# Kernel optimization log

Measured on AMD Instinct MI355X. Metric: run time of the kernel, lower is better.

The kernel has to match this reference:

```python
import math
import jax, jax.numpy as jnp
import numpy as np

NUM_HEADS = 16
HEAD_DIM = 64
MAX_POS = 2048  # max_position_embeddings


def setup_inputs() -> dict:
    key = jax.random.key(0)
    ks = jax.random.split(key, 8)
    B, S, H = 2, 2048, 1024
    return {
        "hidden_states": jax.random.normal(ks[0], (B, S, H), jnp.float32),
        "Wq": jax.random.normal(ks[1], (H, H), jnp.float32) * 0.02,
        "bq": jax.random.normal(ks[2], (H,), jnp.float32) * 0.02,
        "Wk": jax.random.normal(ks[3], (H, H), jnp.float32) * 0.02,
        "bk": jax.random.normal(ks[4], (H,), jnp.float32) * 0.02,
        "Wv": jax.random.normal(ks[5], (H, H), jnp.float32) * 0.02,
        "bv": jax.random.normal(ks[6], (H,), jnp.float32) * 0.02,
        "dist_emb": jax.random.normal(ks[7], (2 * MAX_POS - 1, HEAD_DIM), jnp.float32) * 0.02,
    }


def reference(hidden_states, Wq, bq, Wk, bk, Wv, bv, dist_emb):
    B, S, H = hidden_states.shape
    nh, hd = NUM_HEADS, HEAD_DIM
    # projections (nn.Linear: x @ W.T + b), split into heads
    q = (hidden_states @ Wq.T + bq).reshape(B, S, nh, hd)
    k = (hidden_states @ Wk.T + bk).reshape(B, S, nh, hd)
    v = (hidden_states @ Wv.T + bv).reshape(B, S, nh, hd)
    scale = 1.0 / math.sqrt(hd)
    scores = jnp.einsum('bqhd,bkhd->bhqk', q, k) * scale  # [B,H,S,S]
    # relative position embeddings: distance = q_pos - k_pos
    pos = jnp.arange(S)
    distance = pos[:, None] - pos[None, :]          # [S,S]
    pe = dist_emb[MAX_POS - 1 + distance]           # [S,S,hd]
    rel_q = jnp.einsum('bqhd,qkd->bhqk', q, pe) * scale
    rel_k = jnp.einsum('bkhd,qkd->bhqk', k, pe) * scale
    scores = scores + rel_q + rel_k
    probs = jax.nn.softmax(scores, axis=-1)         # dropout p=0.0
    ctx = jnp.einsum('bhqk,bkhd->bqhd', probs, v)
    return ctx.reshape(B, S, nh * hd)
```

## Files before the change

kernel.cpp:

```cpp
#include <hip/hip_runtime.h>
#include <hip/hip_bf16.h>

#define NH 16
#define HD 64
#define SEQ 2048
#define HID 1024
#define MAXP 2048
#define ST_R 68

typedef float f32x4 __attribute__((ext_vector_type(4)));
typedef short bf16x8 __attribute__((ext_vector_type(8)));
typedef unsigned short u16;
typedef unsigned short u16x8 __attribute__((ext_vector_type(8)));

__device__ __forceinline__ u16 f2bf_hw(float x) {
  union { __hip_bfloat16 h; u16 u; } v;
  v.h = __float2bfloat16(x);
  return v.u;
}
__device__ __forceinline__ unsigned pk2(float a, float b) {
  return (unsigned)f2bf_hw(a) | ((unsigned)f2bf_hw(b) << 16);
}
__device__ __forceinline__ float bf2f(u16 h) {
  union { unsigned u; float f; } v; v.u = ((unsigned)h) << 16;
  return v.f;
}

#define SWZ(r, c) ((r) * 64 + ((((c) >> 3) ^ ((r) & 7)) << 3) + ((c) & 7))

__device__ __forceinline__ void async_copy16(void* lds, const void* g) {
  __builtin_amdgcn_global_load_lds(
      (const __attribute__((address_space(1))) unsigned int*)g,
      (__attribute__((address_space(3))) unsigned int*)lds, 16, 0, 0);
}

__global__ __launch_bounds__(256) void cvt_f32_bf16(
    const float* __restrict__ src, u16* __restrict__ dst, int n4) {
  int i = blockIdx.x * 256 + threadIdx.x;
  const int stride = gridDim.x * 256;
  for (; i < n4; i += stride) {
    const float4 v = reinterpret_cast<const float4*>(src)[i];
    uint2 d;
    d.x = pk2(v.x, v.y);
    d.y = pk2(v.z, v.w);
    reinterpret_cast<uint2*>(dst)[i] = d;
  }
}

__global__ __launch_bounds__(256) void proj_mfma(
    const u16* __restrict__ Xb, const u16* __restrict__ W0,
    const u16* __restrict__ W1, const u16* __restrict__ W2,
    const float* __restrict__ b0, const float* __restrict__ b1,
    const float* __restrict__ b2,
    u16* __restrict__ O0, u16* __restrict__ O1, u16* __restrict__ O2) {
  __shared__ u16 sA[128 * 64];
  __shared__ u16 sB[128 * 64];
  const int t = threadIdx.x, lane = t & 63, w = t >> 6;
  const int g = lane >> 4, li = lane & 15;
  const int wsel = blockIdx.x >> 3;
  const int n0 = (blockIdx.x & 7) * 128, m0 = blockIdx.y * 128;
  const u16* Wb = wsel == 0 ? W0 : (wsel == 1 ? W1 : W2);
  const float* bias = wsel == 0 ? b0 : (wsel == 1 ? b1 : b2);
  u16* Ob = wsel == 0 ? O0 : (wsel == 1 ? O1 : O2);
  const float oscale = wsel == 0 ? 0.125f : 1.0f;
  const int wr = w >> 1, wc = w & 1;

  f32x4 acc[4][4];
#pragma unroll
  for (int i = 0; i < 4; ++i)
#pragma unroll
    for (int j = 0; j < 4; ++j) acc[i][j] = (f32x4)0.0f;

  for (int k0 = 0; k0 < HID; k0 += 64) {
    __syncthreads();
#pragma unroll
    for (int i = 0; i < 4; ++i) {
      const int idx = (w * 4 + i) * 64 + lane;
      const int row = idx >> 3, sch = (idx & 7) ^ (row & 7);
      async_copy16(&sA[(w * 4 + i) * 512], Xb + (size_t)(m0 + row) * HID + k0 + sch * 8);
      async_copy16(&sB[(w * 4 + i) * 512], Wb + (size_t)(n0 + row) * HID + k0 + sch * 8);
    }
    __syncthreads();
    bf16x8 af[4][2], bfr[4][2];
#pragma unroll
    for (int i = 0; i < 4; ++i)
#pragma unroll
      for (int c = 0; c < 2; ++c)
        af[i][c] = *reinterpret_cast<const bf16x8*>(&sA[SWZ(wr * 64 + 16 * i + li, 32 * c + 8 * g)]);
#pragma unroll
    for (int j = 0; j < 4; ++j)
#pragma unroll
      for (int c = 0; c < 2; ++c)
        bfr[j][c] = *reinterpret_cast<const bf16x8*>(&sB[SWZ(wc * 64 + 16 * j + li, 32 * c + 8 * g)]);
#pragma unroll
    for (int i = 0; i < 4; ++i)
#pragma unroll
      for (int j = 0; j < 4; ++j)
#pragma unroll
        for (int c = 0; c < 2; ++c)
          acc[i][j] = __builtin_amdgcn_mfma_f32_16x16x32_bf16(af[i][c], bfr[j][c], acc[i][j], 0, 0, 0);
  }

#pragma unroll
  for (int j = 0; j < 4; ++j) {
    const float bj = bias[n0 + wc * 64 + 16 * j + li];
#pragma unroll
    for (int i = 0; i < 4; ++i)
#pragma unroll
      for (int r = 0; r < 4; ++r)
        Ob[(size_t)(m0 + wr * 64 + 16 * i + 4 * g + r) * HID + n0 + wc * 64 + 16 * j + li] =
            f2bf_hw((acc[i][j][r] + bj) * oscale);
  }
}

__global__ __launch_bounds__(256) void transpose_v(
    const u16* __restrict__ Vin, u16* __restrict__ Vt) {
  __shared__ u16 tile[64 * 65];
  const int t = threadIdx.x;
  const int s0 = blockIdx.x * 64, h = blockIdx.y, b = blockIdx.z;
  const int r = t >> 2, c0 = (t & 3) * 16;
  const u16* gp = Vin + (size_t)(b * SEQ + s0 + r) * HID + h * HD + c0;
  const u16x8 a0 = *reinterpret_cast<const u16x8*>(gp);
  const u16x8 a1 = *reinterpret_cast<const u16x8*>(gp + 8);
#pragma unroll
  for (int i = 0; i < 8; ++i) { tile[r * 65 + c0 + i] = a0[i]; tile[r * 65 + c0 + 8 + i] = a1[i]; }
  __syncthreads();
  const int d = t >> 2, sc = (t & 3) * 16;
  u16x8 o0, o1;
#pragma unroll
  for (int i = 0; i < 8; ++i) {
    o0[i] = tile[(sc + i) * 65 + d];
    o1[i] = tile[(sc + 8 + i) * 65 + d];
  }
  u16* op = Vt + ((size_t)(b * NH + h) * HD + d) * SEQ + s0 + sc;
  *reinterpret_cast<u16x8*>(op) = o0;
  *reinterpret_cast<u16x8*>(op + 8) = o1;
}

__global__ __launch_bounds__(256, 2) void attn_mfma4(
    const u16* __restrict__ Q, const u16* __restrict__ K,
    const u16* __restrict__ Vt, const u16* __restrict__ E,
    float* __restrict__ out) {
  __shared__ u16 sKP[64 * 64];
  __shared__ u16 sV[64 * 64];
  __shared__ u16 sE[128 * 64];
  __shared__ u16 sRq[128 * ST_R];
  __shared__ u16 sRk[128 * ST_R];

  const int t = threadIdx.x;
  const int lane = t & 63, w = t >> 6;
  const int g = lane >> 4, li = lane & 15;
  const int q0 = blockIdx.x * 64;
  const int h = blockIdx.y, b = blockIdx.z;
  const size_t qkbase = (size_t)b * SEQ * HID + (size_t)h * HD;
  const size_t vtbase = (size_t)(b * NH + h) * HD * SEQ;

  bf16x8 qA[2];
#pragma unroll
  for (int c = 0; c < 2; ++c)
    qA[c] = *reinterpret_cast<const bf16x8*>(
        Q + qkbase + (size_t)(q0 + 16 * w + li) * HID + 32 * c + 8 * g);

  f32x4 accO[4];
  float lsum[4];
#pragma unroll
  for (int n = 0; n < 4; ++n) accO[n] = (f32x4)0.0f;
#pragma unroll
  for (int r = 0; r < 4; ++r) lsum[r] = 0.0f;

  const int jb48 = 15 + 16 * w + 4 * g - li;
  const u16* gqp = &sRq[jb48 * ST_R + 16 * w + 4 * g];
  const u16* gkp = &sRk[jb48 * ST_R + li];
  u16* rkw = &sRk[li * ST_R + 16 * w + 4 * g];
  u16* rqw = &sRq[li * ST_R + 16 * w + 4 * g];

  for (int k0 = 0; k0 < SEQ; k0 += 64) {
    const int eb = 1984 + q0 - k0;
    __syncthreads();
#pragma unroll
    for (int i = 0; i < 2; ++i) {
      const int idx = (w * 2 + i) * 64 + lane;
      const int row = idx >> 3, sch = (idx & 7) ^ (row & 7);
      async_copy16(&sKP[(w * 2 + i) * 512], K + qkbase + (size_t)(k0 + row) * HID + sch * 8);
      async_copy16(&sV[(w * 2 + i) * 512], Vt + vtbase + (size_t)row * SEQ + k0 + sch * 8);
    }
#pragma unroll
    for (int i = 0; i < 4; ++i) {
      const int idx = (w * 4 + i) * 64 + lane;
      const int row = idx >> 3, sch = (idx & 7) ^ (row & 7);
      const int er = min(eb + row, 2 * MAXP - 2);
      async_copy16(&sE[(w * 4 + i) * 512], E + (size_t)er * HD + sch * 8);
    }
    __syncthreads();

    bf16x8 kA[2];
#pragma unroll
    for (int c = 0; c < 2; ++c)
      kA[c] = *reinterpret_cast<const bf16x8*>(&sKP[SWZ(16 * w + li, 32 * c + 8 * g)]);
    f32x4 aqk[4];
#pragma unroll
    for (int n = 0; n < 4; ++n) {
      aqk[n] = (f32x4)0.0f;
#pragma unroll
      for (int c = 0; c < 2; ++c) {
        const bf16x8 kB = *reinterpret_cast<const bf16x8*>(&sKP[SWZ(16 * n + li, 32 * c + 8 * g)]);
        aqk[n] = __builtin_amdgcn_mfma_f32_16x16x32_bf16(qA[c], kB, aqk[n], 0, 0, 0);
      }
    }
#pragma unroll
    for (int m = 0; m < 8; ++m) {
      bf16x8 eB[2];
#pragma unroll
      for (int c = 0; c < 2; ++c)
        eB[c] = *reinterpret_cast<const bf16x8*>(&sE[SWZ(16 * m + li, 32 * c + 8 * g)]);
      f32x4 ak = (f32x4)0.0f, aq = (f32x4)0.0f;
#pragma unroll
      for (int c = 0; c < 2; ++c) {
        ak = __builtin_amdgcn_mfma_f32_16x16x32_bf16(kA[c], eB[c], ak, 0, 0, 0);
        aq = __builtin_amdgcn_mfma_f32_16x16x32_bf16(qA[c], eB[c], aq, 0, 0, 0);
      }
      uint2 dk, dq;
      dk.x = pk2(ak[0], ak[1]); dk.y = pk2(ak[2], ak[3]);
      dq.x = pk2(aq[0], aq[1]); dq.y = pk2(aq[2], aq[3]);
      *reinterpret_cast<uint2*>(rkw + m * 16 * ST_R) = dk;
      *reinterpret_cast<uint2*>(rqw + m * 16 * ST_R) = dq;
    }
    __syncthreads();

#pragma unroll
    for (int n = 0; n < 4; ++n)
#pragma unroll
      for (int r = 0; r < 4; ++r) {
        const float relq = bf2f(gqp[(48 + r - 16 * n) * ST_R + r]);
        const float relk = bf2f(gkp[(48 + r - 16 * n) * ST_R + 16 * n]);
        const float p = __expf(fmaf(relk, 0.125f, aqk[n][r] + relq));
        lsum[r] += p;
        sKP[SWZ(16 * w + 4 * g + r, 16 * n + li)] = f2bf_hw(p);
      }
    __syncthreads();

    bf16x8 pA[2];
#pragma unroll
    for (int c = 0; c < 2; ++c)
      pA[c] = *reinterpret_cast<const bf16x8*>(&sKP[SWZ(16 * w + li, 32 * c + 8 * g)]);
#pragma unroll
    for (int n = 0; n < 4; ++n)
#pragma unroll
      for (int c = 0; c < 2; ++c) {
        const bf16x8 vB = *reinterpret_cast<const bf16x8*>(&sV[SWZ(16 * n + li, 32 * c + 8 * g)]);
        accO[n] = __builtin_amdgcn_mfma_f32_16x16x32_bf16(pA[c], vB, accO[n], 0, 0, 0);
      }
  }

#pragma unroll
  for (int off = 1; off < 16; off <<= 1)
#pragma unroll
    for (int r = 0; r < 4; ++r) lsum[r] += __shfl_xor(lsum[r], off, 16);
#pragma unroll
  for (int r = 0; r < 4; ++r) {
    const float inv = 1.0f / lsum[r];
    const size_t row = (size_t)(b * SEQ + q0 + 16 * w + 4 * g + r) * HID + h * HD;
#pragma unroll
    for (int n = 0; n < 4; ++n) out[row + 16 * n + li] = accO[n][r] * inv;
  }
}

extern "C" void kernel_launch(void* const* d_in, const int* in_sizes, int n_in,
                              void* d_out, int out_size, void* d_ws, size_t ws_size,
                              hipStream_t stream) {
  const float* hs = (const float*)d_in[0];
  const float* Wq = (const float*)d_in[1];
  const float* bq = (const float*)d_in[2];
  const float* Wk = (const float*)d_in[3];
  const float* bk = (const float*)d_in[4];
  const float* Wv = (const float*)d_in[5];
  const float* bv = (const float*)d_in[6];
  const float* de = (const float*)d_in[7];
  float* out = (float*)d_out;

  u16* Xb  = (u16*)d_ws;
  u16* Wqb = Xb + (size_t)4194304;
  u16* Wkb = Wqb + (size_t)1048576;
  u16* Wvb = Wkb + (size_t)1048576;
  u16* Qb  = Wvb + (size_t)1048576;
  u16* Kb  = Qb + (size_t)4194304;
  u16* Vb  = Kb + (size_t)4194304;
  u16* Eb  = Vb + (size_t)4194304;
  u16* Vtb = Xb;

  dim3 blk(256);
  hipLaunchKernelGGL(cvt_f32_bf16, dim3(512), blk, 0, stream, hs, Xb, 1048576);
  hipLaunchKernelGGL(cvt_f32_bf16, dim3(256), blk, 0, stream, Wq, Wqb, 262144);
  hipLaunchKernelGGL(cvt_f32_bf16, dim3(256), blk, 0, stream, Wk, Wkb, 262144);
  hipLaunchKernelGGL(cvt_f32_bf16, dim3(256), blk, 0, stream, Wv, Wvb, 262144);
  hipLaunchKernelGGL(cvt_f32_bf16, dim3(128), blk, 0, stream, de, Eb, 65520);

  hipLaunchKernelGGL(proj_mfma, dim3(24, 32), blk, 0, stream,
                     Xb, Wqb, Wkb, Wvb, bq, bk, bv, Qb, Kb, Vb);
  hipLaunchKernelGGL(transpose_v, dim3(SEQ / 64, NH, 2), blk, 0, stream, Vb, Vtb);
  hipLaunchKernelGGL(attn_mfma4, dim3(SEQ / 64, NH, 2), blk, 0, stream, Qb, Kb, Vtb, Eb, out);
}
```

Measured before the change: 264.1 us.

## Double-buffer K tiles and prefetch next distance-embedding tile in attention loop

The attention kernel now keeps two K tiles in shared memory and loads the next K tile while the current one is in use. The next relative-embedding tile is issued right after the mid-loop barrier, so these loads overlap the softmax and PV work. This lets the per-iteration __syncthreads calls drop from four to two raw barriers with explicit waitcnts, and adds s_setprio around the embedding MFMA phase. In exchange it uses more LDS and needs careful manual synchronisation. The final iteration also reads K rows past the end of the sequence.

New measurement: 248.2 us. 1.06x faster.

```diff
diff --git a/kernel.cpp b/kernel.cpp
--- a/kernel.cpp
+++ b/kernel.cpp
@@ -33,6 +33,8 @@
       (const __attribute__((address_space(1))) unsigned int*)g,
       (__attribute__((address_space(3))) unsigned int*)lds, 16, 0, 0);
 }
+__device__ __forceinline__ void vwait0() { asm volatile("s_waitcnt vmcnt(0)" ::: "memory"); }
+__device__ __forceinline__ void lwait0() { asm volatile("s_waitcnt lgkmcnt(0)" ::: "memory"); }
 
 __global__ __launch_bounds__(256) void cvt_f32_bf16(
     const float* __restrict__ src, u16* __restrict__ dst, int n4) {
@@ -137,11 +139,12 @@
   *reinterpret_cast<u16x8*>(op + 8) = o1;
 }
 
-__global__ __launch_bounds__(256, 2) void attn_mfma4(
+__global__ __launch_bounds__(256, 2) void attn_mfma5(
     const u16* __restrict__ Q, const u16* __restrict__ K,
     const u16* __restrict__ Vt, const u16* __restrict__ E,
     float* __restrict__ out) {
-  __shared__ u16 sKP[64 * 64];
+  __shared__ u16 sK0[64 * 64];
+  __shared__ u16 sK1[64 * 64];
   __shared__ u16 sV[64 * 64];
   __shared__ u16 sE[128 * 64];
   __shared__ u16 sRq[128 * ST_R];
@@ -174,39 +177,56 @@
   u16* rkw = &sRk[li * ST_R + 16 * w + 4 * g];
   u16* rqw = &sRq[li * ST_R + 16 * w + 4 * g];
 
+  const int sidx2 = w * 2 * 64 + lane;
+  const int sidx4 = w * 4 * 64 + lane;
+
+  {
+    const int eb0 = 1984 + q0;
+#pragma unroll
+    for (int i = 0; i < 2; ++i) {
+      const int idx = sidx2 + i * 64;
+      const int row = idx >> 3, sch = (idx & 7) ^ (row & 7);
+      async_copy16(&sK0[(w * 2 + i) * 512], K + qkbase + (size_t)row * HID + sch * 8);
+    }
+#pragma unroll
+    for (int i = 0; i < 4; ++i) {
+      const int idx = sidx4 + i * 64;
+      const int row = idx >> 3, sch = (idx & 7) ^ (row & 7);
+      const int er = min(max(eb0 + row, 0), 2 * MAXP - 2);
+      async_copy16(&sE[(w * 4 + i) * 512], E + (size_t)er * HD + sch * 8);
+    }
+    vwait0();
+  }
+
   for (int k0 = 0; k0 < SEQ; k0 += 64) {
-    const int eb = 1984 + q0 - k0;
-    __syncthreads();
+    const int p = (k0 >> 6) & 1;
+    u16* kcur = p ? sK1 : sK0;
+    u16* knxt = p ? sK0 : sK1;
+
+    __builtin_amdgcn_s_barrier();
 #pragma unroll
     for (int i = 0; i < 2; ++i) {
-      const int idx = (w * 2 + i) * 64 + lane;
+      const int idx = sidx2 + i * 64;
       const int row = idx >> 3, sch = (idx & 7) ^ (row & 7);
-      async_copy16(&sKP[(w * 2 + i) * 512], K + qkbase + (size_t)(k0 + row) * HID + sch * 8);
       async_copy16(&sV[(w * 2 + i) * 512], Vt + vtbase + (size_t)row * SEQ + k0 + sch * 8);
-    }
-#pragma unroll
-    for (int i = 0; i < 4; ++i) {
-      const int idx = (w * 4 + i) * 64 + lane;
-      const int row = idx >> 3, sch = (idx & 7) ^ (row & 7);
-      const int er = min(eb + row, 2 * MAXP - 2);
-      async_copy16(&sE[(w * 4 + i) * 512], E + (size_t)er * HD + sch * 8);
-    }
-    __syncthreads();
+      async_copy16(&knxt[(w * 2 + i) * 512], K + qkbase + (size_t)(k0 + 64 + row) * HID + sch * 8);
+    }
 
     bf16x8 kA[2];
 #pragma unroll
     for (int c = 0; c < 2; ++c)
-      kA[c] = *reinterpret_cast<const bf16x8*>(&sKP[SWZ(16 * w + li, 32 * c + 8 * g)]);
+      kA[c] = *reinterpret_cast<const bf16x8*>(&kcur[SWZ(16 * w + li, 32 * c + 8 * g)]);
     f32x4 aqk[4];
 #pragma unroll
     for (int n = 0; n < 4; ++n) {
       aqk[n] = (f32x4)0.0f;
 #pragma unroll
       for (int c = 0; c < 2; ++c) {
-        const bf16x8 kB = *reinterpret_cast<const bf16x8*>(&sKP[SWZ(16 * n + li, 32 * c + 8 * g)]);
+        const bf16x8 kB = *reinterpret_cast<const bf16x8*>(&kcur[SWZ(16 * n + li, 32 * c + 8 * g)]);
         aqk[n] = __builtin_amdgcn_mfma_f32_16x16x32_bf16(qA[c], kB, aqk[n], 0, 0, 0);
       }
     }
+    __builtin_amdgcn_s_setprio(1);
 #pragma unroll
     for (int m = 0; m < 8; ++m) {
       bf16x8 eB[2];
@@ -225,7 +245,22 @@
       *reinterpret_cast<uint2*>(rkw + m * 16 * ST_R) = dk;
       *reinterpret_cast<uint2*>(rqw + m * 16 * ST_R) = dq;
     }
-    __syncthreads();
+    __builtin_amdgcn_s_setprio(0);
+
+    vwait0();
+    lwait0();
+    __builtin_amdgcn_s_barrier();
+
+    {
+      const int ebn = 1920 + q0 - k0;
+#pragma unroll
+      for (int i = 0; i < 4; ++i) {
+        const int idx = sidx4 + i * 64;
+        const int row = idx >> 3, sch = (idx & 7) ^ (row & 7);
+        const int er = min(max(ebn + row, 0), 2 * MAXP - 2);
+        async_copy16(&sE[(w * 4 + i) * 512], E + (size_t)er * HD + sch * 8);
+      }
+    }
 
 #pragma unroll
     for (int n = 0; n < 4; ++n)
@@ -233,16 +268,15 @@
       for (int r = 0; r < 4; ++r) {
         const float relq = bf2f(gqp[(48 + r - 16 * n) * ST_R + r]);
         const float relk = bf2f(gkp[(48 + r - 16 * n) * ST_R + 16 * n]);
-        const float p = __expf(fmaf(relk, 0.125f, aqk[n][r] + relq));
-        lsum[r] += p;
-        sKP[SWZ(16 * w + 4 * g + r, 16 * n + li)] = f2bf_hw(p);
-      }
-    __syncthreads();
+        const float pr = __expf(fmaf(relk, 0.125f, aqk[n][r] + relq));
+        lsum[r] += pr;
+        kcur[SWZ(16 * w + 4 * g + r, 16 * n + li)] = f2bf_hw(pr);
+      }
 
     bf16x8 pA[2];
 #pragma unroll
     for (int c = 0; c < 2; ++c)
-      pA[c] = *reinterpret_cast<const bf16x8*>(&sKP[SWZ(16 * w + li, 32 * c + 8 * g)]);
+      pA[c] = *reinterpret_cast<const bf16x8*>(&kcur[SWZ(16 * w + li, 32 * c + 8 * g)]);
 #pragma unroll
     for (int n = 0; n < 4; ++n)
 #pragma unroll
@@ -250,6 +284,8 @@
         const bf16x8 vB = *reinterpret_cast<const bf16x8*>(&sV[SWZ(16 * n + li, 32 * c + 8 * g)]);
         accO[n] = __builtin_amdgcn_mfma_f32_16x16x32_bf16(pA[c], vB, accO[n], 0, 0, 0);
       }
+
+    vwait0();
   }
 
 #pragma unroll
@@ -298,5 +334,5 @@
   hipLaunchKernelGGL(proj_mfma, dim3(24, 32), blk, 0, stream,
                      Xb, Wqb, Wkb, Wvb, bq, bk, bv, Qb, Kb, Vb);
   hipLaunchKernelGGL(transpose_v, dim3(SEQ / 64, NH, 2), blk, 0, stream, Vb, Vtb);
-  hipLaunchKernelGGL(attn_mfma4, dim3(SEQ / 64, NH, 2), blk, 0, stream, Qb, Kb, Vtb, Eb, out);
-}
+  hipLaunchKernelGGL(attn_mfma5, dim3(SEQ / 64, NH, 2), blk, 0, stream, Qb, Kb, Vtb, Eb, out);
+}
```
